# Kernel tuning notes

Hardware: AMD Instinct MI355X
Metric: run time of the kernel (lower is better)

Reference implementation:

```python
import jax, jax.numpy as jnp
import numpy as np

B, F, S, D = 256, 8, 200, 64
H = 36  # hidden units per field
EPS = 1e-3  # Dice BN epsilon


def setup_inputs() -> dict:
    key0 = jax.random.key(0)
    ks = jax.random.split(key0, 8)
    query = jax.random.normal(ks[0], (B, F, D), dtype=jnp.float32)
    key = jax.random.normal(ks[1], (B, F, S, D), dtype=jnp.float32)
    sequence_num = jax.random.randint(ks[2], (B, F), 1, S + 1, dtype=jnp.int32)
    W_h = jax.random.normal(ks[3], (F, 3 * D, H), dtype=jnp.float32) * 0.05
    b_h = jnp.zeros((F, H), dtype=jnp.float32)
    alpha = jnp.zeros((F,), dtype=jnp.float32)
    W_o = jax.random.normal(ks[4], (F, H, 1), dtype=jnp.float32) * 0.05
    b_o = jnp.zeros((F, 1), dtype=jnp.float32)
    return {"query": query, "key": key, "W_h": W_h, "b_h": b_h,
            "alpha": alpha, "W_o": W_o, "b_o": b_o,
            "sequence_num": sequence_num, "training": 1}


def reference(query, key, W_h, b_h, alpha, W_o, b_o, sequence_num, training):
    # query: [B,F,D], key: [B,F,S,D]
    q = query[:, :, None, :]                      # broadcast instead of tile
    qb = jnp.broadcast_to(q, key.shape)           # [B,F,S,D]
    cat = jnp.concatenate([key, qb, q - key], axis=-1)  # [B,F,S,3D]
    # per-field Dense(36), vectorized across fields
    h = jnp.einsum('bfsc,fch->bfsh', cat, W_h) + b_h[None, :, None, :]
    # Dice: BatchNorm (no affine, training-mode batch stats over batch+seq per field/feature)
    mean = h.mean(axis=(0, 2), keepdims=True)
    var = h.var(axis=(0, 2), keepdims=True)
    p = jax.nn.sigmoid((h - mean) * jax.lax.rsqrt(var + EPS))
    h = (alpha[None, :, None, None] * (1.0 - p) + p) * h
    # per-field Dense(1) -> attention scores [B,F,S]
    scores = jnp.einsum('bfsh,fh->bfs', h, W_o[:, :, 0]) + b_o[None, :, 0, None]
    # mask invalid positions and softmax over sequence
    mask = jnp.arange(key.shape[2])[None, None, :] < sequence_num[:, :, None]
    scores = jnp.where(mask, scores, -jnp.inf)
    attn = jax.nn.softmax(scores, axis=-1)        # [B,F,S]
    # weighted sum over sequence -> [B,F,D]
    return jnp.einsum('bfs,bfsd->bfd', attn, key)
```

## Files before the change

kernel.cpp:

```cpp
#include <hip/hip_runtime.h>
#include <math.h>

#define NB 256
#define NF 8
#define NS 200
#define ND 64
#define NH 36
#define EPSV 1e-3f
#define GRID_BLKS 256

#define WS_SUM 0
#define WS_SQ  288
#define WS_BAR 576

typedef __attribute__((ext_vector_type(8))) short short8;
typedef __attribute__((ext_vector_type(4))) float f32x4;
typedef __attribute__((ext_vector_type(4))) int int4v;

__device__ __forceinline__ unsigned short f32_to_bf16_rne(float x) {
    unsigned u = __float_as_uint(x);
    unsigned r = u + 0x7FFFu + ((u >> 16) & 1u);
    return (unsigned short)(r >> 16);
}
__device__ __forceinline__ float bf16_to_f32(unsigned short h) {
    return __uint_as_float(((unsigned)h) << 16);
}
__device__ __forceinline__ short8 pack8(float4 a, float4 b) {
    int4v t;
    t[0] = (int)__builtin_amdgcn_perm(__float_as_uint(a.y), __float_as_uint(a.x), 0x07060302u);
    t[1] = (int)__builtin_amdgcn_perm(__float_as_uint(a.w), __float_as_uint(a.z), 0x07060302u);
    t[2] = (int)__builtin_amdgcn_perm(__float_as_uint(b.y), __float_as_uint(b.x), 0x07060302u);
    t[3] = (int)__builtin_amdgcn_perm(__float_as_uint(b.w), __float_as_uint(b.z), 0x07060302u);
    return __builtin_bit_cast(short8, t);
}

__global__ __launch_bounds__(512, 2) void k_fused(
    const float* __restrict__ query, const float* __restrict__ key,
    const float* __restrict__ W_h, const float* __restrict__ b_h,
    const float* __restrict__ alpha, const float* __restrict__ W_o,
    const float* __restrict__ b_o, const int* __restrict__ seqn,
    float* __restrict__ ws, float* __restrict__ out)
{
    const int blk = blockIdx.x;
    const int f = blk & (NF - 1);
    const int b0 = (blk >> 3) * 8;
    const int tid = threadIdx.x;
    const int lane = tid & 63;
    const int wv = tid >> 6;
    const int col = lane & 15;
    const int quad = lane >> 4;

    __shared__ __align__(16) unsigned short wkL[48 * 72];
    __shared__ float qs[8][64];
    __shared__ float qts[8][48];
    __shared__ float sumP[48], sqP[48];
    __shared__ float sw[208];
    __shared__ float redM[8], redS[8];
    __shared__ float pout[8][64];

    const float* Wf = W_h + (size_t)f * (3 * ND * NH);
    const size_t bstride = (size_t)NF * NS * ND;
    const float* kb0 = key + (size_t)(b0 * NF + f) * (NS * ND);

    {
        int p = tid >> 6, d = tid & 63;
        qs[p][d] = query[(size_t)((b0 + p) * NF + f) * ND + d];
    }
    for (int i = tid; i < 48 * 64; i += 512) {
        int h = i >> 6, d = i & 63;
        float v = (h < NH) ? (Wf[d * NH + h] - Wf[(2 * ND + d) * NH + h]) : 0.f;
        wkL[h * 72 + d] = f32_to_bf16_rne(v);
    }
    if (tid < 48) { sumP[tid] = 0.f; sqP[tid] = 0.f; }
    __syncthreads();

    if (tid < 384) {
        const int p = tid / 48, hh = tid % 48;
        float acc = 0.f;
        if (hh < NH) {
            acc = b_h[f * NH + hh];
            #pragma unroll 8
            for (int d = 0; d < ND; ++d)
                acc += qs[p][d] * (Wf[(ND + d) * NH + hh] + Wf[(2 * ND + d) * NH + hh]);
        }
        qts[p][hh] = acc;
    }
    short8 bfr[3][2];
    #pragma unroll
    for (int nt = 0; nt < 3; ++nt)
        #pragma unroll
        for (int ks = 0; ks < 2; ++ks)
            bfr[nt][ks] = *(const short8*)&wkL[(nt * 16 + col) * 72 + ks * 32 + quad * 8];
    __syncthreads();

    float s1[3] = {0.f, 0.f, 0.f}, s2[3] = {0.f, 0.f, 0.f};
    float4 Lb[2][2][4];

    auto load_tiles = [&](int j, float4 L[2][4]) {
        const float* kb = kb0 + (size_t)j * bstride;
        #pragma unroll
        for (int i = 0; i < 2; ++i) {
            const int mt = wv + 8 * i;
            if (mt <= 12) {
                const int s = 16 * mt + col;
                const float4* ptr = (const float4*)(kb + (size_t)(s < NS ? s : NS - 1) * ND + quad * 8);
                L[i][0] = ptr[0]; L[i][1] = ptr[1]; L[i][2] = ptr[8]; L[i][3] = ptr[9];
            }
        }
    };

    load_tiles(0, Lb[0]);
    for (int j = 0; j < 8; ++j) {
        if (j < 7) load_tiles(j + 1, Lb[(j + 1) & 1]);
        float4 (*L)[4] = Lb[j & 1];
        const float qv0 = qts[j][col], qv1 = qts[j][16 + col], qv2 = qts[j][32 + col];
        const float qv[3] = {qv0, qv1, qv2};
        #pragma unroll
        for (int i = 0; i < 2; ++i) {
            const int mt = wv + 8 * i;
            if (mt <= 12) {
                short8 fa = pack8(L[i][0], L[i][1]);
                short8 fb = pack8(L[i][2], L[i][3]);
                #pragma unroll
                for (int nt = 0; nt < 3; ++nt) {
                    f32x4 acc = {qv[nt], qv[nt], qv[nt], qv[nt]};
                    acc = __builtin_amdgcn_mfma_f32_16x16x32_bf16(fa, bfr[nt][0], acc, 0, 0, 0);
                    acc = __builtin_amdgcn_mfma_f32_16x16x32_bf16(fb, bfr[nt][1], acc, 0, 0, 0);
                    if (mt < 12) {
                        #pragma unroll
                        for (int r = 0; r < 4; ++r) { float v = acc[r]; s1[nt] += v; s2[nt] += v * v; }
                    } else {
                        const int base_s = 192 + quad * 4;
                        #pragma unroll
                        for (int r = 0; r < 4; ++r)
                            if (base_s + r < NS) { float v = acc[r]; s1[nt] += v; s2[nt] += v * v; }
                    }
                }
            }
        }
    }

    #pragma unroll
    for (int nt = 0; nt < 3; ++nt) {
        float a = s1[nt], c = s2[nt];
        a += __shfl_xor(a, 16, 64); a += __shfl_xor(a, 32, 64);
        c += __shfl_xor(c, 16, 64); c += __shfl_xor(c, 32, 64);
        if (quad == 0) {
            atomicAdd(&sumP[nt * 16 + col], a);
            atomicAdd(&sqP[nt * 16 + col], c);
        }
    }
    __syncthreads();
    if (tid < NH) {
        atomicAdd(&ws[WS_SUM + f * NH + tid], sumP[tid]);
        atomicAdd(&ws[WS_SQ  + f * NH + tid], sqP[tid]);
    }
    __syncthreads();

    if (tid == 0) {
        __threadfence();
        unsigned* cnt = (unsigned*)(ws + WS_BAR);
        __hip_atomic_fetch_add(cnt, 1u, __ATOMIC_ACQ_REL, __HIP_MEMORY_SCOPE_AGENT);
        while (__hip_atomic_load(cnt, __ATOMIC_ACQUIRE, __HIP_MEMORY_SCOPE_AGENT) < (unsigned)GRID_BLKS)
            __builtin_amdgcn_s_sleep(8);
    }
    __syncthreads();

    const float inv_n = 1.f / (float)(NB * NS);
    float mn[3], iv[3], wo[3];
    #pragma unroll
    for (int nt = 0; nt < 3; ++nt) {
        const int hh = nt * 16 + col;
        const bool hv = hh < NH;
        const int hc = hv ? hh : 0;
        const float sm = __hip_atomic_load(&ws[WS_SUM + f * NH + hc], __ATOMIC_RELAXED, __HIP_MEMORY_SCOPE_AGENT);
        const float sq = __hip_atomic_load(&ws[WS_SQ  + f * NH + hc], __ATOMIC_RELAXED, __HIP_MEMORY_SCOPE_AGENT);
        const float m = sm * inv_n;
        mn[nt] = m;
        iv[nt] = rsqrtf(fmaxf(sq * inv_n - m * m, 0.f) + EPSV);
        wo[nt] = hv ? W_o[f * NH + hh] : 0.f;
    }
    const float alf = alpha[f];
    const float bo = b_o[f];

    for (int j = 0; j < 8; ++j) {
        const int bfi = (b0 + j) * NF + f;
        const float* kb = kb0 + (size_t)j * bstride;
        const int sq_n = seqn[bfi];
        const float qv[3] = {qts[j][col], qts[j][16 + col], qts[j][32 + col]};

        short8 kah[2][2];
        #pragma unroll
        for (int i = 0; i < 2; ++i) {
            const int mt = wv + 8 * i;
            if (mt <= 12) {
                const int s = 16 * mt + col;
                const float4* ptr = (const float4*)(kb + (size_t)(s < NS ? s : NS - 1) * ND + quad * 8);
                float4 a0 = ptr[0], a1 = ptr[1], c0 = ptr[8], c1 = ptr[9];
                kah[i][0] = pack8(a0, a1);
                kah[i][1] = pack8(c0, c1);
                float part[4] = {0.f, 0.f, 0.f, 0.f};
                #pragma unroll
                for (int nt = 0; nt < 3; ++nt) {
                    f32x4 acc = {qv[nt], qv[nt], qv[nt], qv[nt]};
                    acc = __builtin_amdgcn_mfma_f32_16x16x32_bf16(kah[i][0], bfr[nt][0], acc, 0, 0, 0);
                    acc = __builtin_amdgcn_mfma_f32_16x16x32_bf16(kah[i][1], bfr[nt][1], acc, 0, 0, 0);
                    #pragma unroll
                    for (int r = 0; r < 4; ++r) {
                        const float h = acc[r];
                        const float pg = 1.f / (1.f + __expf(-(h - mn[nt]) * iv[nt]));
                        part[r] += (alf + (1.f - alf) * pg) * h * wo[nt];
                    }
                }
                #pragma unroll
                for (int r = 0; r < 4; ++r) {
                    float v = part[r];
                    v += __shfl_xor(v, 1, 64); v += __shfl_xor(v, 2, 64);
                    v += __shfl_xor(v, 4, 64); v += __shfl_xor(v, 8, 64);
                    const int srow = 16 * mt + quad * 4 + r;
                    if (col == 0 && srow < NS) sw[srow] = v + bo;
                }
            }
        }
        __syncthreads();

        const bool valid = (tid < NS) && (tid < sq_n);
        const float sc = valid ? sw[tid] : -1e30f;
        float m = sc;
        m = fmaxf(m, __shfl_xor(m, 1, 64));  m = fmaxf(m, __shfl_xor(m, 2, 64));
        m = fmaxf(m, __shfl_xor(m, 4, 64));  m = fmaxf(m, __shfl_xor(m, 8, 64));
        m = fmaxf(m, __shfl_xor(m, 16, 64)); m = fmaxf(m, __shfl_xor(m, 32, 64));
        if (lane == 0) redM[wv] = m;
        __syncthreads();
        float maxv = redM[0];
        #pragma unroll
        for (int w = 1; w < 8; ++w) maxv = fmaxf(maxv, redM[w]);
        const float e = valid ? __expf(sc - maxv) : 0.f;
        float l = e;
        l += __shfl_xor(l, 1, 64);  l += __shfl_xor(l, 2, 64);
        l += __shfl_xor(l, 4, 64);  l += __shfl_xor(l, 8, 64);
        l += __shfl_xor(l, 16, 64); l += __shfl_xor(l, 32, 64);
        if (lane == 0) redS[wv] = l;
        __syncthreads();
        float tot = redS[0];
        #pragma unroll
        for (int w = 1; w < 8; ++w) tot += redS[w];
        const float isum = 1.f / tot;
        if (tid < 208) sw[tid] = e * isum;
        __syncthreads();

        float po0[8] = {0,0,0,0,0,0,0,0}, po1[8] = {0,0,0,0,0,0,0,0};
        #pragma unroll
        for (int i = 0; i < 2; ++i) {
            const int mt = wv + 8 * i;
            if (mt <= 12) {
                const float w = sw[16 * mt + col];
                #pragma unroll
                for (int jj = 0; jj < 8; ++jj) {
                    po0[jj] += w * bf16_to_f32((unsigned short)kah[i][0][jj]);
                    po1[jj] += w * bf16_to_f32((unsigned short)kah[i][1][jj]);
                }
            }
        }
        #pragma unroll
        for (int off = 1; off <= 8; off <<= 1) {
            #pragma unroll
            for (int jj = 0; jj < 8; ++jj) {
                po0[jj] += __shfl_xor(po0[jj], off, 64);
                po1[jj] += __shfl_xor(po1[jj], off, 64);
            }
        }
        if (col == 0) {
            #pragma unroll
            for (int jj = 0; jj < 8; ++jj) {
                pout[wv][quad * 8 + jj] = po0[jj];
                pout[wv][32 + quad * 8 + jj] = po1[jj];
            }
        }
        __syncthreads();
        if (tid < 64) {
            float o = 0.f;
            #pragma unroll
            for (int w = 0; w < 8; ++w) o += pout[w][tid];
            out[(size_t)bfi * ND + tid] = o;
        }
        __syncthreads();
    }
}

extern "C" void kernel_launch(void* const* d_in, const int* in_sizes, int n_in,
                              void* d_out, int out_size, void* d_ws, size_t ws_size,
                              hipStream_t stream) {
    const float* query = (const float*)d_in[0];
    const float* key   = (const float*)d_in[1];
    const float* W_h   = (const float*)d_in[2];
    const float* b_h   = (const float*)d_in[3];
    const float* alpha = (const float*)d_in[4];
    const float* W_o   = (const float*)d_in[5];
    const float* b_o   = (const float*)d_in[6];
    const int*   seqn  = (const int*)d_in[7];
    float* out = (float*)d_out;
    float* ws  = (float*)d_ws;

    hipMemsetAsync(ws, 0, 578 * sizeof(float), stream);
    k_fused<<<GRID_BLKS, 512, 0, stream>>>(query, key, W_h, b_h, alpha, W_o, b_o, seqn, ws, out);
}
```

Before: 249.9 us.

## Split fused grid-barrier kernel into stats and attention kernels with per-row blocks

Replaces the single persistent kernel, which used a software grid barrier over 256 blocks of 512 threads, with two launches of 2048 small blocks, one per (batch, field) row. The stats kernel leaves the query term out of the MFMA accumulator and folds it into the sums analytically. It also stores the per-row query projection in the workspace so the attention kernel can reuse it. The attention kernel does the final weighted sum over keys in full fp32, reloading key from memory instead of reusing the bf16 copy held in registers. This removes the spin barrier and raises parallelism, at the cost of an extra launch, recomputing the bf16 weight prep in every block, and reading key a third time.

```diff
diff --git a/kernel.cpp b/kernel.cpp
--- a/kernel.cpp
+++ b/kernel.cpp
@@ -7,11 +7,10 @@
 #define ND 64
 #define NH 36
 #define EPSV 1e-3f
-#define GRID_BLKS 256
 
 #define WS_SUM 0
 #define WS_SQ  288
-#define WS_BAR 576
+#define WS_QT  1152
 
 typedef __attribute__((ext_vector_type(8))) short short8;
 typedef __attribute__((ext_vector_type(4))) float f32x4;
@@ -21,9 +20,6 @@
     unsigned u = __float_as_uint(x);
     unsigned r = u + 0x7FFFu + ((u >> 16) & 1u);
     return (unsigned short)(r >> 16);
-}
-__device__ __forceinline__ float bf16_to_f32(unsigned short h) {
-    return __uint_as_float(((unsigned)h) << 16);
 }
 __device__ __forceinline__ short8 pack8(float4 a, float4 b) {
     int4v t;
@@ -34,147 +30,151 @@
     return __builtin_bit_cast(short8, t);
 }
 
-__global__ __launch_bounds__(512, 2) void k_fused(
+__global__ __launch_bounds__(128, 4) void k_stats(
     const float* __restrict__ query, const float* __restrict__ key,
     const float* __restrict__ W_h, const float* __restrict__ b_h,
-    const float* __restrict__ alpha, const float* __restrict__ W_o,
-    const float* __restrict__ b_o, const int* __restrict__ seqn,
-    float* __restrict__ ws, float* __restrict__ out)
+    float* __restrict__ ws)
 {
     const int blk = blockIdx.x;
     const int f = blk & (NF - 1);
-    const int b0 = (blk >> 3) * 8;
     const int tid = threadIdx.x;
-    const int lane = tid & 63;
-    const int wv = tid >> 6;
-    const int col = lane & 15;
-    const int quad = lane >> 4;
+    const int lane = tid & 63, wv = tid >> 6;
+    const int col = lane & 15, quad = lane >> 4;
 
     __shared__ __align__(16) unsigned short wkL[48 * 72];
-    __shared__ float qs[8][64];
-    __shared__ float qts[8][48];
-    __shared__ float sumP[48], sqP[48];
-    __shared__ float sw[208];
-    __shared__ float redM[8], redS[8];
-    __shared__ float pout[8][64];
+    __shared__ float qsL[64];
+    __shared__ float qtL[48];
+    __shared__ float s1L[2][48], s2L[2][48];
 
     const float* Wf = W_h + (size_t)f * (3 * ND * NH);
-    const size_t bstride = (size_t)NF * NS * ND;
-    const float* kb0 = key + (size_t)(b0 * NF + f) * (NS * ND);
-
+    const float* kbase = key + (size_t)blk * (NS * ND);
+
+    float4 cur[4], nxt[4];
     {
-        int p = tid >> 6, d = tid & 63;
-        qs[p][d] = query[(size_t)((b0 + p) * NF + f) * ND + d];
-    }
-    for (int i = tid; i < 48 * 64; i += 512) {
+        const int s = min(16 * wv + col, NS - 1);
+        const float4* p = (const float4*)(kbase + (size_t)s * ND + quad * 8);
+        cur[0] = p[0]; cur[1] = p[1]; cur[2] = p[8]; cur[3] = p[9];
+    }
+    if (tid < 64) qsL[tid] = query[(size_t)blk * ND + tid];
+    for (int i = tid; i < 48 * 64; i += 128) {
         int h = i >> 6, d = i & 63;
         float v = (h < NH) ? (Wf[d * NH + h] - Wf[(2 * ND + d) * NH + h]) : 0.f;
         wkL[h * 72 + d] = f32_to_bf16_rne(v);
     }
-    if (tid < 48) { sumP[tid] = 0.f; sqP[tid] = 0.f; }
-    __syncthreads();
-
-    if (tid < 384) {
-        const int p = tid / 48, hh = tid % 48;
-        float acc = 0.f;
-        if (hh < NH) {
-            acc = b_h[f * NH + hh];
-            #pragma unroll 8
-            for (int d = 0; d < ND; ++d)
-                acc += qs[p][d] * (Wf[(ND + d) * NH + hh] + Wf[(2 * ND + d) * NH + hh]);
-        }
-        qts[p][hh] = acc;
-    }
+    __syncthreads();
+
     short8 bfr[3][2];
     #pragma unroll
     for (int nt = 0; nt < 3; ++nt)
         #pragma unroll
         for (int ks = 0; ks < 2; ++ks)
             bfr[nt][ks] = *(const short8*)&wkL[(nt * 16 + col) * 72 + ks * 32 + quad * 8];
-    __syncthreads();
 
     float s1[3] = {0.f, 0.f, 0.f}, s2[3] = {0.f, 0.f, 0.f};
-    float4 Lb[2][2][4];
-
-    auto load_tiles = [&](int j, float4 L[2][4]) {
-        const float* kb = kb0 + (size_t)j * bstride;
-        #pragma unroll
-        for (int i = 0; i < 2; ++i) {
-            const int mt = wv + 8 * i;
-            if (mt <= 12) {
-                const int s = 16 * mt + col;
-                const float4* ptr = (const float4*)(kb + (size_t)(s < NS ? s : NS - 1) * ND + quad * 8);
-                L[i][0] = ptr[0]; L[i][1] = ptr[1]; L[i][2] = ptr[8]; L[i][3] = ptr[9];
+    #pragma unroll
+    for (int t = 0; t < 7; ++t) {
+        const int mt = wv + 2 * t;
+        if (t < 6) {
+            const int sn = min(16 * (mt + 2) + col, NS - 1);
+            const float4* p = (const float4*)(kbase + (size_t)sn * ND + quad * 8);
+            nxt[0] = p[0]; nxt[1] = p[1]; nxt[2] = p[8]; nxt[3] = p[9];
+        }
+        const short8 fa = pack8(cur[0], cur[1]);
+        const short8 fb = pack8(cur[2], cur[3]);
+        const int base_s = 16 * mt + quad * 4;
+        #pragma unroll
+        for (int nt = 0; nt < 3; ++nt) {
+            f32x4 acc = {0.f, 0.f, 0.f, 0.f};
+            acc = __builtin_amdgcn_mfma_f32_16x16x32_bf16(fa, bfr[nt][0], acc, 0, 0, 0);
+            acc = __builtin_amdgcn_mfma_f32_16x16x32_bf16(fb, bfr[nt][1], acc, 0, 0, 0);
+            #pragma unroll
+            for (int r = 0; r < 4; ++r) {
+                const float v = (base_s + r < NS) ? acc[r] : 0.f;
+                s1[nt] += v; s2[nt] += v * v;
             }
         }
-    };
-
-    load_tiles(0, Lb[0]);
-    for (int j = 0; j < 8; ++j) {
-        if (j < 7) load_tiles(j + 1, Lb[(j + 1) & 1]);
-        float4 (*L)[4] = Lb[j & 1];
-        const float qv0 = qts[j][col], qv1 = qts[j][16 + col], qv2 = qts[j][32 + col];
-        const float qv[3] = {qv0, qv1, qv2};
-        #pragma unroll
-        for (int i = 0; i < 2; ++i) {
-            const int mt = wv + 8 * i;
-            if (mt <= 12) {
-                short8 fa = pack8(L[i][0], L[i][1]);
-                short8 fb = pack8(L[i][2], L[i][3]);
-                #pragma unroll
-                for (int nt = 0; nt < 3; ++nt) {
-                    f32x4 acc = {qv[nt], qv[nt], qv[nt], qv[nt]};
-                    acc = __builtin_amdgcn_mfma_f32_16x16x32_bf16(fa, bfr[nt][0], acc, 0, 0, 0);
-                    acc = __builtin_amdgcn_mfma_f32_16x16x32_bf16(fb, bfr[nt][1], acc, 0, 0, 0);
-                    if (mt < 12) {
-                        #pragma unroll
-                        for (int r = 0; r < 4; ++r) { float v = acc[r]; s1[nt] += v; s2[nt] += v * v; }
-                    } else {
-                        const int base_s = 192 + quad * 4;
-                        #pragma unroll
-                        for (int r = 0; r < 4; ++r)
-                            if (base_s + r < NS) { float v = acc[r]; s1[nt] += v; s2[nt] += v * v; }
-                    }
-                }
-            }
-        }
-    }
+        cur[0] = nxt[0]; cur[1] = nxt[1]; cur[2] = nxt[2]; cur[3] = nxt[3];
+    }
+
+    if (tid >= 64 && tid < 64 + NH) {
+        const int h = tid - 64;
+        float acc = b_h[f * NH + h];
+        #pragma unroll 8
+        for (int d = 0; d < ND; ++d)
+            acc += qsL[d] * (Wf[(ND + d) * NH + h] + Wf[(2 * ND + d) * NH + h]);
+        qtL[h] = acc;
+        ws[WS_QT + (size_t)blk * 48 + h] = acc;
+    }
+    if (tid >= 64 + NH && tid < 64 + 48)
+        ws[WS_QT + (size_t)blk * 48 + (tid - 64)] = 0.f;
 
     #pragma unroll
     for (int nt = 0; nt < 3; ++nt) {
         float a = s1[nt], c = s2[nt];
         a += __shfl_xor(a, 16, 64); a += __shfl_xor(a, 32, 64);
         c += __shfl_xor(c, 16, 64); c += __shfl_xor(c, 32, 64);
-        if (quad == 0) {
-            atomicAdd(&sumP[nt * 16 + col], a);
-            atomicAdd(&sqP[nt * 16 + col], c);
-        }
+        if (quad == 0) { s1L[wv][nt * 16 + col] = a; s2L[wv][nt * 16 + col] = c; }
     }
     __syncthreads();
     if (tid < NH) {
-        atomicAdd(&ws[WS_SUM + f * NH + tid], sumP[tid]);
-        atomicAdd(&ws[WS_SQ  + f * NH + tid], sqP[tid]);
-    }
-    __syncthreads();
-
-    if (tid == 0) {
-        __threadfence();
-        unsigned* cnt = (unsigned*)(ws + WS_BAR);
-        __hip_atomic_fetch_add(cnt, 1u, __ATOMIC_ACQ_REL, __HIP_MEMORY_SCOPE_AGENT);
-        while (__hip_atomic_load(cnt, __ATOMIC_ACQUIRE, __HIP_MEMORY_SCOPE_AGENT) < (unsigned)GRID_BLKS)
-            __builtin_amdgcn_s_sleep(8);
-    }
-    __syncthreads();
+        const float S1 = s1L[0][tid] + s1L[1][tid];
+        const float S2 = s2L[0][tid] + s2L[1][tid];
+        const float qt = qtL[tid];
+        atomicAdd(&ws[WS_SUM + f * NH + tid], S1 + 200.f * qt);
+        atomicAdd(&ws[WS_SQ  + f * NH + tid], S2 + 2.f * qt * S1 + 200.f * qt * qt);
+    }
+}
+
+__global__ __launch_bounds__(128, 4) void k_attn(
+    const float* __restrict__ key, const float* __restrict__ W_h,
+    const float* __restrict__ alpha, const float* __restrict__ W_o,
+    const float* __restrict__ b_o, const int* __restrict__ seqn,
+    const float* __restrict__ ws, float* __restrict__ out)
+{
+    const int blk = blockIdx.x;
+    const int f = blk & (NF - 1);
+    const int tid = threadIdx.x;
+    const int lane = tid & 63, wv = tid >> 6;
+    const int col = lane & 15, quad = lane >> 4;
+
+    __shared__ __align__(16) unsigned short wkL[48 * 72];
+    __shared__ float swL[208];
+    __shared__ float redA[2], redB[2];
+    __shared__ float poutL[2][64];
+
+    const float* Wf = W_h + (size_t)f * (3 * ND * NH);
+    const float* kbase = key + (size_t)blk * (NS * ND);
+
+    float4 cur[4], nxt[4];
+    {
+        const int s = min(16 * wv + col, NS - 1);
+        const float4* p = (const float4*)(kbase + (size_t)s * ND + quad * 8);
+        cur[0] = p[0]; cur[1] = p[1]; cur[2] = p[8]; cur[3] = p[9];
+    }
+    for (int i = tid; i < 48 * 64; i += 128) {
+        int h = i >> 6, d = i & 63;
+        float v = (h < NH) ? (Wf[d * NH + h] - Wf[(2 * ND + d) * NH + h]) : 0.f;
+        wkL[h * 72 + d] = f32_to_bf16_rne(v);
+    }
+    __syncthreads();
+
+    short8 bfr[3][2];
+    #pragma unroll
+    for (int nt = 0; nt < 3; ++nt)
+        #pragma unroll
+        for (int ks = 0; ks < 2; ++ks)
+            bfr[nt][ks] = *(const short8*)&wkL[(nt * 16 + col) * 72 + ks * 32 + quad * 8];
 
     const float inv_n = 1.f / (float)(NB * NS);
-    float mn[3], iv[3], wo[3];
+    float qv[3], mn[3], iv[3], wo[3];
     #pragma unroll
     for (int nt = 0; nt < 3; ++nt) {
         const int hh = nt * 16 + col;
         const bool hv = hh < NH;
         const int hc = hv ? hh : 0;
-        const float sm = __hip_atomic_load(&ws[WS_SUM + f * NH + hc], __ATOMIC_RELAXED, __HIP_MEMORY_SCOPE_AGENT);
-        const float sq = __hip_atomic_load(&ws[WS_SQ  + f * NH + hc], __ATOMIC_RELAXED, __HIP_MEMORY_SCOPE_AGENT);
+        qv[nt] = ws[WS_QT + (size_t)blk * 48 + hh];
+        const float sm = ws[WS_SUM + f * NH + hc];
+        const float sq = ws[WS_SQ  + f * NH + hc];
         const float m = sm * inv_n;
         mn[nt] = m;
         iv[nt] = rsqrtf(fmaxf(sq * inv_n - m * m, 0.f) + EPSV);
@@ -182,110 +182,78 @@
     }
     const float alf = alpha[f];
     const float bo = b_o[f];
-
-    for (int j = 0; j < 8; ++j) {
-        const int bfi = (b0 + j) * NF + f;
-        const float* kb = kb0 + (size_t)j * bstride;
-        const int sq_n = seqn[bfi];
-        const float qv[3] = {qts[j][col], qts[j][16 + col], qts[j][32 + col]};
-
-        short8 kah[2][2];
-        #pragma unroll
-        for (int i = 0; i < 2; ++i) {
-            const int mt = wv + 8 * i;
-            if (mt <= 12) {
-                const int s = 16 * mt + col;
-                const float4* ptr = (const float4*)(kb + (size_t)(s < NS ? s : NS - 1) * ND + quad * 8);
-                float4 a0 = ptr[0], a1 = ptr[1], c0 = ptr[8], c1 = ptr[9];
-                kah[i][0] = pack8(a0, a1);
-                kah[i][1] = pack8(c0, c1);
-                float part[4] = {0.f, 0.f, 0.f, 0.f};
-                #pragma unroll
-                for (int nt = 0; nt < 3; ++nt) {
-                    f32x4 acc = {qv[nt], qv[nt], qv[nt], qv[nt]};
-                    acc = __builtin_amdgcn_mfma_f32_16x16x32_bf16(kah[i][0], bfr[nt][0], acc, 0, 0, 0);
-                    acc = __builtin_amdgcn_mfma_f32_16x16x32_bf16(kah[i][1], bfr[nt][1], acc, 0, 0, 0);
-                    #pragma unroll
-                    for (int r = 0; r < 4; ++r) {
-                        const float h = acc[r];
-                        const float pg = 1.f / (1.f + __expf(-(h - mn[nt]) * iv[nt]));
-                        part[r] += (alf + (1.f - alf) * pg) * h * wo[nt];
-                    }
-                }
-                #pragma unroll
-                for (int r = 0; r < 4; ++r) {
-                    float v = part[r];
-                    v += __shfl_xor(v, 1, 64); v += __shfl_xor(v, 2, 64);
-                    v += __shfl_xor(v, 4, 64); v += __shfl_xor(v, 8, 64);
-                    const int srow = 16 * mt + quad * 4 + r;
-                    if (col == 0 && srow < NS) sw[srow] = v + bo;
-                }
+    const int sq_n = seqn[blk];
+
+    #pragma unroll
+    for (int t = 0; t < 7; ++t) {
+        const int mt = wv + 2 * t;
+        if (t < 6) {
+            const int sn = min(16 * (mt + 2) + col, NS - 1);
+            const float4* p = (const float4*)(kbase + (size_t)sn * ND + quad * 8);
+            nxt[0] = p[0]; nxt[1] = p[1]; nxt[2] = p[8]; nxt[3] = p[9];
+        }
+        const short8 fa = pack8(cur[0], cur[1]);
+        const short8 fb = pack8(cur[2], cur[3]);
+        float part[4] = {0.f, 0.f, 0.f, 0.f};
+        #pragma unroll
+        for (int nt = 0; nt < 3; ++nt) {
+            f32x4 acc = {qv[nt], qv[nt], qv[nt], qv[nt]};
+            acc = __builtin_amdgcn_mfma_f32_16x16x32_bf16(fa, bfr[nt][0], acc, 0, 0, 0);
+            acc = __builtin_amdgcn_mfma_f32_16x16x32_bf16(fb, bfr[nt][1], acc, 0, 0, 0);
+            #pragma unroll
+            for (int r = 0; r < 4; ++r) {
+                const float h = acc[r];
+                const float pg = 1.f / (1.f + __expf(-(h - mn[nt]) * iv[nt]));
+                part[r] += (alf + (1.f - alf) * pg) * h * wo[nt];
             }
         }
-        __syncthreads();
-
-        const bool valid = (tid < NS) && (tid < sq_n);
-        const float sc = valid ? sw[tid] : -1e30f;
-        float m = sc;
-        m = fmaxf(m, __shfl_xor(m, 1, 64));  m = fmaxf(m, __shfl_xor(m, 2, 64));
-        m = fmaxf(m, __shfl_xor(m, 4, 64));  m = fmaxf(m, __shfl_xor(m, 8, 64));
-        m = fmaxf(m, __shfl_xor(m, 16, 64)); m = fmaxf(m, __shfl_xor(m, 32, 64));
-        if (lane == 0) redM[wv] = m;
-        __syncthreads();
-        float maxv = redM[0];
-        #pragma unroll
-        for (int w = 1; w < 8; ++w) maxv = fmaxf(maxv, redM[w]);
-        const float e = valid ? __expf(sc - maxv) : 0.f;
-        float l = e;
-        l += __shfl_xor(l, 1, 64);  l += __shfl_xor(l, 2, 64);
-        l += __shfl_xor(l, 4, 64);  l += __shfl_xor(l, 8, 64);
-        l += __shfl_xor(l, 16, 64); l += __shfl_xor(l, 32, 64);
-        if (lane == 0) redS[wv] = l;
-        __syncthreads();
-        float tot = redS[0];
-        #pragma unroll
-        for (int w = 1; w < 8; ++w) tot += redS[w];
-        const float isum = 1.f / tot;
-        if (tid < 208) sw[tid] = e * isum;
-        __syncthreads();
-
-        float po0[8] = {0,0,0,0,0,0,0,0}, po1[8] = {0,0,0,0,0,0,0,0};
-        #pragma unroll
-        for (int i = 0; i < 2; ++i) {
-            const int mt = wv + 8 * i;
-            if (mt <= 12) {
-                const float w = sw[16 * mt + col];
-                #pragma unroll
-                for (int jj = 0; jj < 8; ++jj) {
-                    po0[jj] += w * bf16_to_f32((unsigned short)kah[i][0][jj]);
-                    po1[jj] += w * bf16_to_f32((unsigned short)kah[i][1][jj]);
-                }
-            }
-        }
-        #pragma unroll
-        for (int off = 1; off <= 8; off <<= 1) {
-            #pragma unroll
-            for (int jj = 0; jj < 8; ++jj) {
-                po0[jj] += __shfl_xor(po0[jj], off, 64);
-                po1[jj] += __shfl_xor(po1[jj], off, 64);
-            }
-        }
-        if (col == 0) {
-            #pragma unroll
-            for (int jj = 0; jj < 8; ++jj) {
-                pout[wv][quad * 8 + jj] = po0[jj];
-                pout[wv][32 + quad * 8 + jj] = po1[jj];
-            }
-        }
-        __syncthreads();
-        if (tid < 64) {
-            float o = 0.f;
-            #pragma unroll
-            for (int w = 0; w < 8; ++w) o += pout[w][tid];
-            out[(size_t)bfi * ND + tid] = o;
-        }
-        __syncthreads();
-    }
+        #pragma unroll
+        for (int r = 0; r < 4; ++r) {
+            float v = part[r];
+            v += __shfl_xor(v, 1, 64); v += __shfl_xor(v, 2, 64);
+            v += __shfl_xor(v, 4, 64); v += __shfl_xor(v, 8, 64);
+            const int srow = 16 * mt + quad * 4 + r;
+            if (col == 0 && srow < NS) swL[srow] = v + bo;
+        }
+        cur[0] = nxt[0]; cur[1] = nxt[1]; cur[2] = nxt[2]; cur[3] = nxt[3];
+    }
+    __syncthreads();
+
+    const int i2 = tid + 128;
+    const float v1 = (tid < sq_n) ? swL[tid] : -1e30f;
+    const float v2 = (i2 < NS && i2 < sq_n) ? swL[i2] : -1e30f;
+    float m = fmaxf(v1, v2);
+    m = fmaxf(m, __shfl_xor(m, 1, 64));  m = fmaxf(m, __shfl_xor(m, 2, 64));
+    m = fmaxf(m, __shfl_xor(m, 4, 64));  m = fmaxf(m, __shfl_xor(m, 8, 64));
+    m = fmaxf(m, __shfl_xor(m, 16, 64)); m = fmaxf(m, __shfl_xor(m, 32, 64));
+    if (lane == 0) redA[wv] = m;
+    __syncthreads();
+    const float maxv = fmaxf(redA[0], redA[1]);
+    const float e1 = (tid < sq_n) ? __expf(v1 - maxv) : 0.f;
+    const float e2 = (i2 < NS && i2 < sq_n) ? __expf(v2 - maxv) : 0.f;
+    float l = e1 + e2;
+    l += __shfl_xor(l, 1, 64);  l += __shfl_xor(l, 2, 64);
+    l += __shfl_xor(l, 4, 64);  l += __shfl_xor(l, 8, 64);
+    l += __shfl_xor(l, 16, 64); l += __shfl_xor(l, 32, 64);
+    if (lane == 0) redB[wv] = l;
+    __syncthreads();
+    const float isum = 1.f / (redB[0] + redB[1]);
+    swL[tid] = e1 * isum;
+    if (i2 < 208) swL[i2] = e2 * isum;
+    __syncthreads();
+
+    {
+        const int d = lane;
+        float acc = 0.f;
+        const int s0 = wv * 100;
+        #pragma unroll 10
+        for (int s = s0; s < s0 + 100; ++s)
+            acc += swL[s] * kbase[(size_t)s * ND + d];
+        poutL[wv][d] = acc;
+    }
+    __syncthreads();
+    if (tid < 64)
+        out[(size_t)blk * ND + tid] = poutL[0][tid] + poutL[1][tid];
 }
 
 extern "C" void kernel_launch(void* const* d_in, const int* in_sizes, int n_in,
@@ -302,6 +270,7 @@
     float* out = (float*)d_out;
     float* ws  = (float*)d_ws;
 
-    hipMemsetAsync(ws, 0, 578 * sizeof(float), stream);
-    k_fused<<<GRID_BLKS, 512, 0, stream>>>(query, key, W_h, b_h, alpha, W_o, b_o, seqn, ws, out);
-}
+    hipMemsetAsync(ws, 0, 576 * sizeof(float), stream);
+    k_stats<<<NB * NF, 128, 0, stream>>>(query, key, W_h, b_h, ws);
+    k_attn<<<NB * NF, 128, 0, stream>>>(key, W_h, alpha, W_o, b_o, seqn, ws, out);
+}
```

Measured after the change: 225.7 us. 1.11x faster.
